# Optimization experiments

Hardware: AMD Instinct MI355X
Metric: run time of the kernel (lower is better)

The kernel has to match this reference:

```python
import jax, jax.numpy as jnp
import numpy as np

N_NODES = 100000
N_EDGES = 1600000
IN_CH = 48
OUT_CH = 64
K = 2


def setup_inputs() -> dict:
    key = jax.random.key(0)
    k1, k2, k3, k4 = jax.random.split(key, 4)
    x = jax.random.normal(k1, (N_NODES, IN_CH), dtype=jnp.float32)
    edge_index = jax.random.randint(k2, (2, N_EDGES), 0, N_NODES, dtype=jnp.int64)
    W = jax.random.normal(k3, (IN_CH, OUT_CH), dtype=jnp.float32) * (1.0 / np.sqrt(IN_CH))
    b = jax.random.normal(k4, (OUT_CH,), dtype=jnp.float32) * 0.01
    return {"x": x, "edge_index": edge_index, "W": W, "b": b}


def _propagate(x, row, col):
    n = x.shape[0]
    # degree of each node counted over col (destination) indices
    deg = jax.ops.segment_sum(jnp.ones_like(col, dtype=x.dtype), col, num_segments=n)
    deg_inv_sqrt = jnp.where(deg > 0, jax.lax.rsqrt(jnp.where(deg > 0, deg, 1.0)), 0.0)
    norm = deg_inv_sqrt[row] * deg_inv_sqrt[col]  # [E]
    # gather-scale-scatter: out[col] += x[row] * norm
    msgs = x[row] * norm[:, None]  # [E, d]
    return jax.ops.segment_sum(msgs, col, num_segments=n)


def reference(x, edge_index, W, b):
    row, col = edge_index[0], edge_index[1]
    h = x
    for _ in range(K):
        h = _propagate(h, row, col)
    return h @ W + b
```

## Files before the change

### kernel.cpp

```cpp
#include <hip/hip_runtime.h>
#include <hip/hip_bf16.h>
#include <hip/hip_fp16.h>


#define N_NODES 100000
#define N_EDGES 1600000
#define IN_CH 48
#define OUT_CH 64
#define NBUCKETS 392
#define CAP 4608
#define EPB 8192
#define NBLK_EDGE 196
#define NBLK_BKT 391

__global__ void init_kernel(int* __restrict__ bucketCursor, int* __restrict__ binTotal) {
    int t = threadIdx.x;
    if (t < NBUCKETS) bucketCursor[t] = t * CAP;
    if (t < 64) binTotal[t] = 0;
}

__global__ void bucket_scatter_kernel(const int* __restrict__ row, const int* __restrict__ col,
                                      int* __restrict__ bucketCursor, int* __restrict__ edge_packed) {
    __shared__ int lh[NBUCKETS];
    __shared__ int lofs[NBUCKETS];
    __shared__ int lbase[NBUCKETS];
    __shared__ int stage[EPB];
    __shared__ unsigned short sbkt[EPB];
    __shared__ int wsum[4];
    int tid = threadIdx.x;
    int base = blockIdx.x * EPB;
    for (int i = tid; i < NBUCKETS; i += 256) lh[i] = 0;
    __syncthreads();
    #pragma unroll 4
    for (int k = 0; k < 32; k++) {
        int e = base + k * 256 + tid;
        if (e < N_EDGES) atomicAdd(&lh[col[e] >> 8], 1);
    }
    __syncthreads();
    {
        int c0 = (tid < 196) ? lh[2 * tid] : 0;
        int c1 = (tid < 196) ? lh[2 * tid + 1] : 0;
        int s = c0 + c1;
        int incl = s;
        int lane = tid & 63, w = tid >> 6;
        #pragma unroll
        for (int o = 1; o < 64; o <<= 1) {
            int v = __shfl_up(incl, o, 64);
            if (lane >= o) incl += v;
        }
        if (lane == 63) wsum[w] = incl;
        __syncthreads();
        int wbase = 0;
        for (int k = 0; k < w; k++) wbase += wsum[k];
        int ex = wbase + incl - s;
        if (tid < 196) {
            lofs[2 * tid]     = ex;
            lofs[2 * tid + 1] = ex + c0;
        }
    }
    __syncthreads();
    for (int i = tid; i < NBUCKETS; i += 256) {
        int c = lh[i];
        if (c > 0) lbase[i] = atomicAdd(&bucketCursor[i], c);
        lh[i] = 0;
    }
    __syncthreads();
    #pragma unroll 4
    for (int k = 0; k < 32; k++) {
        int e = base + k * 256 + tid;
        if (e < N_EDGES) {
            int c = col[e];
            int bkt = c >> 8;
            int r = atomicAdd(&lh[bkt], 1);
            int slot = lofs[bkt] + r;
            stage[slot] = (row[e] << 8) | (c & 255);
            sbkt[slot] = (unsigned short)bkt;
        }
    }
    __syncthreads();
    int total = (base + EPB <= N_EDGES) ? EPB : (N_EDGES - base);
    for (int i = tid; i < total; i += 256) {
        int bkt = sbkt[i];
        int dst = lbase[bkt] + (i - lofs[bkt]);
        if (dst < (bkt + 1) * CAP)
            edge_packed[dst] = stage[i];
    }
}

__global__ void fine_sort_kernel(const int* __restrict__ edge_packed,
                                 const int* __restrict__ bucketCursor,
                                 const float* __restrict__ x,
                                 int* __restrict__ edge_src,
                                 int* __restrict__ deg, int* __restrict__ start,
                                 float* __restrict__ dis, int* __restrict__ binTotal,
                                 __half2* __restrict__ xs) {
    __shared__ int fh[256];
    __shared__ int sfh[257];
    __shared__ int cur[256];
    __shared__ int bh[64];
    __shared__ float fdis[256];
    int b = blockIdx.x;
    int t = threadIdx.x;
    int s0 = b * CAP;
    int s1 = min(bucketCursor[b], (b + 1) * CAP);
    int nodeBase = b << 8;
    fh[t] = 0;
    if (t < 64) bh[t] = 0;
    __syncthreads();
    for (int j = s0 + t; j < s1; j += 256)
        atomicAdd(&fh[edge_packed[j] & 255], 1);
    __syncthreads();
    if (t == 0) {
        int s = 0;
        for (int k = 0; k < 256; k++) { sfh[k] = s; s += fh[k]; }
        sfh[256] = s;
    }
    __syncthreads();
    int node = nodeBase + t;
    bool valid = (node < N_NODES);
    int d = fh[t];
    float dv = (valid && d > 0) ? rsqrtf((float)d) : 0.0f;
    cur[t] = sfh[t];
    fdis[t] = dv;
    if (valid) {
        deg[node] = d;
        start[node] = s0 + sfh[t];
        dis[node] = dv;
        atomicAdd(&bh[min(d, 63)], 1);
    }
    __syncthreads();
    for (int i = t; i < 256 * 24; i += 256) {
        int ln = i / 24;
        int nd = nodeBase + ln;
        if (nd < N_NODES) {
            int ci = i - ln * 24;
            float dd = fdis[ln];
            float2 v = ((const float2*)x)[nd * 24 + ci];
            xs[nd * 24 + ci] = __floats2half2_rn(v.x * dd, v.y * dd);
        }
    }
    for (int j = s0 + t; j < s1; j += 256) {
        int rc = edge_packed[j];
        int p = atomicAdd(&cur[rc & 255], 1);
        edge_src[s0 + p] = rc >> 8;
    }
    __syncthreads();
    if (t < 64 && bh[t]) atomicAdd(&binTotal[t], bh[t]);
}

__global__ void binscan_kernel(const int* __restrict__ binTotal, int* __restrict__ binCursor) {
    if (threadIdx.x == 0) {
        int s = 0;
        for (int k = 63; k >= 0; k--) { binCursor[k] = s; s += binTotal[k]; }
    }
}

__global__ void order_kernel(const int* __restrict__ deg, const int* __restrict__ start,
                             const float* __restrict__ dis, int* __restrict__ binCursor,
                             int4* __restrict__ nodeinfo, int n) {
    __shared__ int lhist[64];
    __shared__ int lbase[64];
    int i = blockIdx.x * 256 + threadIdx.x;
    if (threadIdx.x < 64) lhist[threadIdx.x] = 0;
    __syncthreads();
    int bin = 0, myrank = 0;
    if (i < n) {
        bin = min(deg[i], 63);
        myrank = atomicAdd(&lhist[bin], 1);
    }
    __syncthreads();
    if (threadIdx.x < 64 && lhist[threadIdx.x] > 0)
        lbase[threadIdx.x] = atomicAdd(&binCursor[threadIdx.x], lhist[threadIdx.x]);
    __syncthreads();
    if (i < n)
        nodeinfo[lbase[bin] + myrank] = make_int4(i, start[i], deg[i], __float_as_int(dis[i]));
}

#define LOAD3(p, v0, v1, v2) { v0 = (p)[0]; v1 = (p)[1]; v2 = (p)[2]; }
#define ACC6(v0, v1, v2) { \
    float2 u0 = __half22float2(v0), u1 = __half22float2(v1), u2 = __half22float2(v2); \
    a0 += u0.x; a1 += u0.y; a2 += u1.x; a3 += u1.y; a4 += u2.x; a5 += u2.y; }
#define ACC6B(v0, v1, v2) { \
    float2 u0 = __half22float2(v0), u1 = __half22float2(v1), u2 = __half22float2(v2); \
    b0 += u0.x; b1 += u0.y; b2 += u1.x; b3 += u1.y; b4 += u2.x; b5 += u2.y; }

__global__ void gather1_kernel(const __half2* __restrict__ xs,
                               const int* __restrict__ edge_src,
                               const int4* __restrict__ nodeinfo,
                               __half2* __restrict__ h1) {
    int g = blockIdx.x * 32 + (threadIdx.x >> 3);
    int lane = threadIdx.x & 7;
    int4 ni = nodeinfo[g];
    int node = ni.x, s = ni.y, e = s + ni.z;
    float dv = __int_as_float(ni.w);
    float a0 = 0, a1 = 0, a2 = 0, a3 = 0, a4 = 0, a5 = 0;
    float b0 = 0, b1 = 0, b2 = 0, b3 = 0, b4 = 0, b5 = 0;
    int j = s;
    for (; j + 3 < e; j += 4) {
        int s0 = edge_src[j], s1 = edge_src[j + 1], s2 = edge_src[j + 2], s3 = edge_src[j + 3];
        const __half2* p0 = xs + s0 * 24 + lane * 3;
        const __half2* p1 = xs + s1 * 24 + lane * 3;
        const __half2* p2 = xs + s2 * 24 + lane * 3;
        const __half2* p3 = xs + s3 * 24 + lane * 3;
        __half2 v00,v01,v02, v10,v11,v12, v20,v21,v22, v30,v31,v32;
        LOAD3(p0, v00, v01, v02); LOAD3(p1, v10, v11, v12);
        LOAD3(p2, v20, v21, v22); LOAD3(p3, v30, v31, v32);
        ACC6(v00, v01, v02); ACC6B(v10, v11, v12);
        ACC6(v20, v21, v22); ACC6B(v30, v31, v32);
    }
    for (; j < e; ++j) {
        const __half2* p0 = xs + edge_src[j] * 24 + lane * 3;
        __half2 v00, v01, v02;
        LOAD3(p0, v00, v01, v02);
        ACC6(v00, v01, v02);
    }
    a0 += b0; a1 += b1; a2 += b2; a3 += b3; a4 += b4; a5 += b5;
    float sc = dv * dv;
    __half2* q = h1 + node * 24 + lane * 3;
    q[0] = __floats2half2_rn(a0 * sc, a1 * sc);
    q[1] = __floats2half2_rn(a2 * sc, a3 * sc);
    q[2] = __floats2half2_rn(a4 * sc, a5 * sc);
}

__global__ void gather2_gemm_kernel(const __half2* __restrict__ h1,
                                    const int* __restrict__ edge_src,
                                    const int4* __restrict__ nodeinfo,
                                    const float* __restrict__ W,
                                    const float* __restrict__ bias,
                                    float* __restrict__ out) {
    __shared__ float sW[IN_CH * OUT_CH];
    __shared__ float sb[OUT_CH];
    __shared__ float sh[32][IN_CH + 1];

    for (int i = threadIdx.x; i < IN_CH * OUT_CH; i += 256) sW[i] = W[i];
    if (threadIdx.x < OUT_CH) sb[threadIdx.x] = bias[threadIdx.x];

    int nl = threadIdx.x >> 3;
    int lane = threadIdx.x & 7;
    int g = blockIdx.x * 32 + nl;
    int4 ni = nodeinfo[g];
    int node = ni.x, s = ni.y, e = s + ni.z;
    float dv = __int_as_float(ni.w);

    float a0 = 0, a1 = 0, a2 = 0, a3 = 0, a4 = 0, a5 = 0;
    float b0 = 0, b1 = 0, b2 = 0, b3 = 0, b4 = 0, b5 = 0;
    int j = s;
    for (; j + 3 < e; j += 4) {
        int s0 = edge_src[j], s1 = edge_src[j + 1], s2 = edge_src[j + 2], s3 = edge_src[j + 3];
        const __half2* p0 = h1 + s0 * 24 + lane * 3;
        const __half2* p1 = h1 + s1 * 24 + lane * 3;
        const __half2* p2 = h1 + s2 * 24 + lane * 3;
        const __half2* p3 = h1 + s3 * 24 + lane * 3;
        __half2 v00,v01,v02, v10,v11,v12, v20,v21,v22, v30,v31,v32;
        LOAD3(p0, v00, v01, v02); LOAD3(p1, v10, v11, v12);
        LOAD3(p2, v20, v21, v22); LOAD3(p3, v30, v31, v32);
        ACC6(v00, v01, v02); ACC6B(v10, v11, v12);
        ACC6(v20, v21, v22); ACC6B(v30, v31, v32);
    }
    for (; j < e; ++j) {
        const __half2* p0 = h1 + edge_src[j] * 24 + lane * 3;
        __half2 v00, v01, v02;
        LOAD3(p0, v00, v01, v02);
        ACC6(v00, v01, v02);
    }
    a0 += b0; a1 += b1; a2 += b2; a3 += b3; a4 += b4; a5 += b5;
    int c0 = 6 * lane;
    sh[nl][c0 + 0] = a0 * dv;
    sh[nl][c0 + 1] = a1 * dv;
    sh[nl][c0 + 2] = a2 * dv;
    sh[nl][c0 + 3] = a3 * dv;
    sh[nl][c0 + 4] = a4 * dv;
    sh[nl][c0 + 5] = a5 * dv;
    __syncthreads();

    int j0 = lane * 8;
    float acc[8];
    #pragma unroll
    for (int i = 0; i < 8; i++) acc[i] = sb[j0 + i];
    for (int k = 0; k < IN_CH; k++) {
        float s0 = sh[nl][k];
        #pragma unroll
        for (int i = 0; i < 8; i++) acc[i] += s0 * sW[k * OUT_CH + j0 + i];
    }
    float4* o = (float4*)(out + (size_t)node * OUT_CH + j0);
    o[0] = make_float4(acc[0], acc[1], acc[2], acc[3]);
    o[1] = make_float4(acc[4], acc[5], acc[6], acc[7]);
}

extern "C" void kernel_launch(void* const* d_in, const int* in_sizes, int n_in,
                              void* d_out, int out_size, void* d_ws, size_t ws_size,
                              hipStream_t stream) {
    const float* x   = (const float*)d_in[0];
    const int*   ei  = (const int*)d_in[1];
    const float* W   = (const float*)d_in[2];
    const float* b   = (const float*)d_in[3];
    float* out = (float*)d_out;

    const int* row = ei;
    const int* col = ei + N_EDGES;

    int* ws_i = (int*)d_ws;
    int* bucketCursor = ws_i;
    int* binTotal     = ws_i + 512;
    int* binCursor    = ws_i + 576;
    int* deg          = ws_i + 1024;
    int* start        = ws_i + 101376;
    float* dis        = (float*)(ws_i + 201728);
    int4* nodeinfo    = (int4*)(ws_i + 302080);
    int* edge_packed  = ws_i + 703488;
    int* edge_src     = ws_i + 2509824;
    __half2* xs       = (__half2*)(ws_i + 4316160);
    __half2* h1       = (__half2*)(ws_i + 6716160);

    init_kernel<<<1, 512, 0, stream>>>(bucketCursor, binTotal);
    bucket_scatter_kernel<<<NBLK_EDGE, 256, 0, stream>>>(row, col, bucketCursor, edge_packed);
    fine_sort_kernel<<<NBLK_BKT, 256, 0, stream>>>(edge_packed, bucketCursor, x,
                                                   edge_src, deg, start, dis, binTotal, xs);
    binscan_kernel<<<1, 64, 0, stream>>>(binTotal, binCursor);
    order_kernel<<<(N_NODES + 255) / 256, 256, 0, stream>>>(deg, start, dis, binCursor,
                                                            nodeinfo, N_NODES);

    gather1_kernel<<<N_NODES / 32, 256, 0, stream>>>(xs, edge_src, nodeinfo, h1);
    gather2_gemm_kernel<<<N_NODES / 32, 256, 0, stream>>>(h1, edge_src, nodeinfo, W, b, out);
}
```

Before: 232.0 us.

## Cache bucket ranks in registers and stage fine sort through shared memory

The bucket scatter kernel now records each edge's column, bucket and local rank in per-thread arrays during the histogram pass. This removes the second pass of col reloads and shared atomics. The fine sort kernel loads each bucket's packed edges into shared memory once, does the counting-sort placement there, and writes edge_src back contiguously instead of as scattered global stores. The costs are 32-entry register arrays per thread (spill risk) and about 36KB more LDS in fine_sort, which is given a launch bound of 256 threads and 2 blocks.

```diff
diff --git a/kernel.cpp b/kernel.cpp
--- a/kernel.cpp
+++ b/kernel.cpp
@@ -29,12 +29,23 @@
     __shared__ int wsum[4];
     int tid = threadIdx.x;
     int base = blockIdx.x * EPB;
+    int myrank[32];
+    int mybkt[32];
+    int mycol[32];
     for (int i = tid; i < NBUCKETS; i += 256) lh[i] = 0;
     __syncthreads();
     #pragma unroll 4
     for (int k = 0; k < 32; k++) {
         int e = base + k * 256 + tid;
-        if (e < N_EDGES) atomicAdd(&lh[col[e] >> 8], 1);
+        if (e < N_EDGES) {
+            int c = col[e];
+            int bkt = c >> 8;
+            mycol[k] = c;
+            mybkt[k] = bkt;
+            myrank[k] = atomicAdd(&lh[bkt], 1);
+        } else {
+            mybkt[k] = -1;
+        }
     }
     __syncthreads();
     {
@@ -62,18 +73,15 @@
     for (int i = tid; i < NBUCKETS; i += 256) {
         int c = lh[i];
         if (c > 0) lbase[i] = atomicAdd(&bucketCursor[i], c);
-        lh[i] = 0;
     }
     __syncthreads();
     #pragma unroll 4
     for (int k = 0; k < 32; k++) {
-        int e = base + k * 256 + tid;
-        if (e < N_EDGES) {
-            int c = col[e];
-            int bkt = c >> 8;
-            int r = atomicAdd(&lh[bkt], 1);
-            int slot = lofs[bkt] + r;
-            stage[slot] = (row[e] << 8) | (c & 255);
+        int bkt = mybkt[k];
+        if (bkt >= 0) {
+            int e = base + k * 256 + tid;
+            int slot = lofs[bkt] + myrank[k];
+            stage[slot] = (row[e] << 8) | (mycol[k] & 255);
             sbkt[slot] = (unsigned short)bkt;
         }
     }
@@ -87,13 +95,16 @@
     }
 }
 
-__global__ void fine_sort_kernel(const int* __restrict__ edge_packed,
-                                 const int* __restrict__ bucketCursor,
-                                 const float* __restrict__ x,
-                                 int* __restrict__ edge_src,
-                                 int* __restrict__ deg, int* __restrict__ start,
-                                 float* __restrict__ dis, int* __restrict__ binTotal,
-                                 __half2* __restrict__ xs) {
+__global__ void __launch_bounds__(256, 2)
+fine_sort_kernel(const int* __restrict__ edge_packed,
+                 const int* __restrict__ bucketCursor,
+                 const float* __restrict__ x,
+                 int* __restrict__ edge_src,
+                 int* __restrict__ deg, int* __restrict__ start,
+                 float* __restrict__ dis, int* __restrict__ binTotal,
+                 __half2* __restrict__ xs) {
+    __shared__ int ein[CAP];
+    __shared__ int eout[CAP];
     __shared__ int fh[256];
     __shared__ int sfh[257];
     __shared__ int cur[256];
@@ -102,13 +113,16 @@
     int b = blockIdx.x;
     int t = threadIdx.x;
     int s0 = b * CAP;
-    int s1 = min(bucketCursor[b], (b + 1) * CAP);
+    int cnt = min(bucketCursor[b], (b + 1) * CAP) - s0;
     int nodeBase = b << 8;
     fh[t] = 0;
     if (t < 64) bh[t] = 0;
     __syncthreads();
-    for (int j = s0 + t; j < s1; j += 256)
-        atomicAdd(&fh[edge_packed[j] & 255], 1);
+    for (int j = t; j < cnt; j += 256) {
+        int rc = edge_packed[s0 + j];
+        ein[j] = rc;
+        atomicAdd(&fh[rc & 255], 1);
+    }
     __syncthreads();
     if (t == 0) {
         int s = 0;
@@ -129,6 +143,11 @@
         atomicAdd(&bh[min(d, 63)], 1);
     }
     __syncthreads();
+    for (int j = t; j < cnt; j += 256) {
+        int rc = ein[j];
+        int p = atomicAdd(&cur[rc & 255], 1);
+        eout[p] = rc >> 8;
+    }
     for (int i = t; i < 256 * 24; i += 256) {
         int ln = i / 24;
         int nd = nodeBase + ln;
@@ -139,12 +158,8 @@
             xs[nd * 24 + ci] = __floats2half2_rn(v.x * dd, v.y * dd);
         }
     }
-    for (int j = s0 + t; j < s1; j += 256) {
-        int rc = edge_packed[j];
-        int p = atomicAdd(&cur[rc & 255], 1);
-        edge_src[s0 + p] = rc >> 8;
-    }
-    __syncthreads();
+    __syncthreads();
+    for (int j = t; j < cnt; j += 256) edge_src[s0 + j] = eout[j];
     if (t < 64 && bh[t]) atomicAdd(&binTotal[t], bh[t]);
 }
 
```

New measurement: 238.3 us. 1.03x slower.
